# Kernel optimization log

Hardware: AMD Instinct MI355X
Metric: run time of the kernel (lower is better)

The kernel has to match this reference:

```python
import jax, jax.numpy as jnp
import numpy as np

B, T, D = 2, 2048, 2048
H, DH, DR, DL = 16, 128, 64, 512
WINDOW, STRIDE, GLOBAL = 512, 64, 128
BASE, MAX_SEQ, ORIG_MAX = 10000.0, 131072, 4096
BETA_FAST, BETA_SLOW = 32.0, 1.0
SCALE = 1.0 / np.sqrt(DH)
SCALE_ROPE = 1.0 / np.sqrt(DR)


def _yarn_inv_freq():
    base_inv = 1.0 / (BASE ** (np.arange(0, DR, 2, dtype=np.float32) / DR))
    scale = MAX_SEQ / ORIG_MAX
    freqs = np.arange(DR // 2, dtype=np.float32)
    ramp = np.clip((freqs - BETA_SLOW) / (BETA_FAST - BETA_SLOW), 0.0, 1.0)
    return jnp.asarray(base_inv * (1 - ramp) + (base_inv / scale) * ramp)

_INV_FREQ = _yarn_inv_freq()
_YARN_FACTOR = np.float32(0.1 * np.log(MAX_SEQ / ORIG_MAX) + 1.0)


def _apply_rope(x):
    # x: [B, H, T, DR]
    t = jnp.arange(x.shape[2], dtype=jnp.float32)
    fr = t[:, None] * _INV_FREQ[None, :]            # [T, DR/2]
    emb = jnp.concatenate([fr, fr], axis=-1)        # [T, DR]
    cos, sin = jnp.cos(emb), jnp.sin(emb)
    x1, x2 = jnp.split(x, 2, axis=-1)
    rot = jnp.concatenate([-x2, x1], axis=-1)
    return (x * cos + rot * sin) * _YARN_FACTOR


def _sparse_mask(seq_len):
    pos = jnp.arange(seq_len)
    qp, kp = pos[:, None], pos[None, :]
    dist = qp - kp
    half = WINDOW // 2
    window = (dist >= -half) & (dist <= half)
    dilated = (kp % STRIDE == 0) | (kp < GLOBAL)
    causal = kp <= qp
    return (window | dilated) & causal              # [T, T] bool


def setup_inputs() -> dict:
    key = jax.random.key(0)
    ks = jax.random.split(key, 9)
    s = 0.02
    return {
        "x": jax.random.normal(ks[0], (B, T, D), jnp.float32),
        "w_q": jax.random.normal(ks[1], (D, D), jnp.float32) * s,
        "w_dkv": jax.random.normal(ks[2], (D, DL), jnp.float32) * s,
        "w_uk": jax.random.normal(ks[3], (DL, D), jnp.float32) * s,
        "w_uv": jax.random.normal(ks[4], (DL, D), jnp.float32) * s,
        "w_q_pos": jax.random.normal(ks[5], (D, H * DR), jnp.float32) * s,
        "w_k_pos": jax.random.normal(ks[6], (D, H * DR), jnp.float32) * s,
        "w_o": jax.random.normal(ks[7], (D, D), jnp.float32) * s,
    }


def reference(x, w_q, w_dkv, w_uk, w_uv, w_q_pos, w_k_pos, w_o):
    b, t, _ = x.shape
    # MLA projections
    q_c = (x @ w_q).reshape(b, t, H, DH).transpose(0, 2, 1, 3)      # [B,H,T,DH]
    c_kv = x @ w_dkv                                                # [B,T,DL]
    k_c = (c_kv @ w_uk).reshape(b, t, H, DH).transpose(0, 2, 1, 3)
    v_c = (c_kv @ w_uv).reshape(b, t, H, DH).transpose(0, 2, 1, 3)
    # decoupled RoPE branch (YaRN)
    q_r = (x @ w_q_pos).reshape(b, t, H, DR).transpose(0, 2, 1, 3)
    k_r = (x @ w_k_pos).reshape(b, t, H, DR).transpose(0, 2, 1, 3)
    q_r = _apply_rope(q_r)
    k_r = _apply_rope(k_r)
    # combined content + positional scores
    scores = jnp.einsum("bhqd,bhkd->bhqk", q_c, k_c) * SCALE \
           + jnp.einsum("bhqr,bhkr->bhqk", q_r, k_r) * SCALE_ROPE
    mask = _sparse_mask(t)                                          # [T,T]
    scores = jnp.where(mask[None, None], scores, -jnp.inf)
    attn = jax.nn.softmax(scores, axis=-1)
    out = jnp.einsum("bhqk,bhkd->bhqd", attn, v_c)                  # [B,H,T,DH]
    out = out.transpose(0, 2, 1, 3).reshape(b, t, D)
    return out @ w_o
```

## Files before the change

kernel.cpp:

```cpp
#include <hip/hip_runtime.h>
#include <hip/hip_bf16.h>
#include <cstdint>

typedef __attribute__((ext_vector_type(8))) short short8_t;
typedef __attribute__((ext_vector_type(4))) short short4_t;
typedef __attribute__((ext_vector_type(4))) float f32x4_t;

#define AS1 __attribute__((address_space(1)))
#define AS3 __attribute__((address_space(3)))

__device__ __forceinline__ void gload_lds16(const void* g, void* l) {
  __builtin_amdgcn_global_load_lds((const AS1 void*)g, (AS3 void*)l, 16, 0, 0);
}

__device__ __forceinline__ short8_t ld8(const __hip_bfloat16* p) {
  return *(const short8_t*)p;
}

__global__ __launch_bounds__(256) void k_convert(const float* __restrict__ in,
                                                 __hip_bfloat16* __restrict__ out, int n) {
  int i = (blockIdx.x * 256 + threadIdx.x) * 8;
  if (i >= n) return;
  union { short8_t v; __hip_bfloat16 h[8]; } u;
#pragma unroll
  for (int j = 0; j < 8; ++j) u.h[j] = __float2bfloat16(in[i + j]);
  *(short8_t*)(out + i) = u.v;
}

__global__ __launch_bounds__(256) void k_transpose(const float* __restrict__ in,
                                                   __hip_bfloat16* __restrict__ out,
                                                   int R, int C) {
  __shared__ float t[64][65];
  int nct = C >> 6;
  int ct = blockIdx.x % nct, rt = blockIdx.x / nct;
  int r0 = rt << 6, c0 = ct << 6;
#pragma unroll
  for (int i = 0; i < 16; ++i) {
    int idx = i * 256 + threadIdx.x;
    int r = idx >> 6, c = idx & 63;
    t[r][c] = in[(size_t)(r0 + r) * C + c0 + c];
  }
  __syncthreads();
#pragma unroll
  for (int i = 0; i < 16; ++i) {
    int idx = i * 256 + threadIdx.x;
    int c = idx >> 6, r = idx & 63;
    out[(size_t)(c0 + c) * R + r0 + r] = __float2bfloat16(t[r][c]);
  }
}

template<int OUT_F32>
__global__ __launch_bounds__(256) void k_gemm_bt(const __hip_bfloat16* __restrict__ A,
                                                 const __hip_bfloat16* __restrict__ Bt,
                                                 void* __restrict__ C,
                                                 int M, int N, int K, float alpha) {
  __shared__ __align__(16) __hip_bfloat16 Al[128 * 32];
  __shared__ __align__(16) __hip_bfloat16 Bl[128 * 32];
  int nbx = N >> 7;
  int bx = blockIdx.x % nbx, by = blockIdx.x / nbx;
  int tid = threadIdx.x, lane = tid & 63, w = tid >> 6;
  int wr = (w >> 1) << 6, wc = (w & 1) << 6;
  f32x4_t acc[4][4] = {};
  const __hip_bfloat16* Ag = A + (size_t)(by * 128) * K;
  const __hip_bfloat16* Bg = Bt + (size_t)(bx * 128) * K;
  int srow = w * 32 + (lane >> 2);
  int scol = (lane & 3) * 8;
  for (int k0 = 0; k0 < K; k0 += 32) {
    __syncthreads();
    gload_lds16(Ag + (size_t)srow * K + k0 + scol,        Al + (w * 32) * 32);
    gload_lds16(Ag + (size_t)(srow + 16) * K + k0 + scol, Al + (w * 32 + 16) * 32);
    gload_lds16(Bg + (size_t)srow * K + k0 + scol,        Bl + (w * 32) * 32);
    gload_lds16(Bg + (size_t)(srow + 16) * K + k0 + scol, Bl + (w * 32 + 16) * 32);
    __syncthreads();
    short8_t af[4], bf[4];
#pragma unroll
    for (int m = 0; m < 4; ++m)
      af[m] = ld8(Al + (wr + 16 * m + (lane & 15)) * 32 + 8 * (lane >> 4));
#pragma unroll
    for (int n = 0; n < 4; ++n)
      bf[n] = ld8(Bl + (wc + 16 * n + (lane & 15)) * 32 + 8 * (lane >> 4));
#pragma unroll
    for (int m = 0; m < 4; ++m)
#pragma unroll
      for (int n = 0; n < 4; ++n)
        acc[m][n] = __builtin_amdgcn_mfma_f32_16x16x32_bf16(af[m], bf[n], acc[m][n], 0, 0, 0);
  }
  int r0 = by * 128 + wr + 4 * (lane >> 4);
  int c0 = bx * 128 + wc + (lane & 15);
#pragma unroll
  for (int m = 0; m < 4; ++m)
#pragma unroll
    for (int n = 0; n < 4; ++n)
#pragma unroll
      for (int i = 0; i < 4; ++i) {
        size_t o = (size_t)(r0 + 16 * m + i) * N + c0 + 16 * n;
        float v = acc[m][n][i] * alpha;
        if (OUT_F32) ((float*)C)[o] = v;
        else ((__hip_bfloat16*)C)[o] = __float2bfloat16(v);
      }
}

__global__ __launch_bounds__(256) void k_gemm_proj1(const __hip_bfloat16* __restrict__ A,
                                                    const __hip_bfloat16* __restrict__ Bt,
                                                    __hip_bfloat16* __restrict__ qcb,
                                                    __hip_bfloat16* __restrict__ qrb,
                                                    __hip_bfloat16* __restrict__ krb,
                                                    __hip_bfloat16* __restrict__ ckv) {
  const int K = 2048;
  __shared__ __align__(16) __hip_bfloat16 Al[128 * 32];
  __shared__ __align__(16) __hip_bfloat16 Bl[128 * 32];
  int bx = blockIdx.x % 36, by = blockIdx.x / 36;
  int tid = threadIdx.x, lane = tid & 63, w = tid >> 6;
  int L = lane & 15, hi = lane >> 4;
  int wr = (w >> 1) << 6, wc = (w & 1) << 6;
  f32x4_t acc[4][4] = {};
  const __hip_bfloat16* Ag = A + (size_t)(by * 128) * K;
  const __hip_bfloat16* Bg = Bt + (size_t)(bx * 128) * K;
  int srow = w * 32 + (lane >> 2);
  int scol = (lane & 3) * 8;
  for (int k0 = 0; k0 < K; k0 += 32) {
    __syncthreads();
    gload_lds16(Ag + (size_t)srow * K + k0 + scol,        Al + (w * 32) * 32);
    gload_lds16(Ag + (size_t)(srow + 16) * K + k0 + scol, Al + (w * 32 + 16) * 32);
    gload_lds16(Bg + (size_t)srow * K + k0 + scol,        Bl + (w * 32) * 32);
    gload_lds16(Bg + (size_t)(srow + 16) * K + k0 + scol, Bl + (w * 32 + 16) * 32);
    __syncthreads();
    short8_t af[4], bf[4];
#pragma unroll
    for (int m = 0; m < 4; ++m)
      af[m] = ld8(Al + (wr + 16 * m + L) * 32 + 8 * hi);
#pragma unroll
    for (int n = 0; n < 4; ++n)
      bf[n] = ld8(Bl + (wc + 16 * n + L) * 32 + 8 * hi);
#pragma unroll
    for (int m = 0; m < 4; ++m)
#pragma unroll
      for (int n = 0; n < 4; ++n)
        acc[m][n] = __builtin_amdgcn_mfma_f32_16x16x32_bf16(af[m], bf[n], acc[m][n], 0, 0, 0);
  }
  int r0 = by * 128 + wr + 4 * hi;
  int cb = bx * 128 + wc;
  if (bx < 16) {
    const float SCALE = 0.08838834764831845f;
#pragma unroll
    for (int m = 0; m < 4; ++m)
#pragma unroll
      for (int n = 0; n < 4; ++n)
#pragma unroll
        for (int i = 0; i < 4; ++i)
          qcb[(size_t)(r0 + 16 * m + i) * 2048 + cb + 16 * n + L] =
              __float2bfloat16(acc[m][n][i] * SCALE);
  } else if (bx < 32) {
    bool isq = bx < 24;
    __hip_bfloat16* dst = isq ? qrb : krb;
    float osc = isq ? 0.16832169878499666f : 1.3465735902799727f;
    int cbl = cb - (isq ? 2048 : 3072);
    float invf[2];
#pragma unroll
    for (int p = 0; p < 2; ++p) {
      float fi = (float)(16 * p + L);
      float bi = __expf(fi * -0.28782313662425574f);
      float ramp = fminf(fmaxf((fi - 1.0f) * (1.0f / 31.0f), 0.0f), 1.0f);
      invf[p] = bi * (1.0f - ramp * (31.0f / 32.0f));
    }
#pragma unroll
    for (int m = 0; m < 4; ++m)
#pragma unroll
      for (int i = 0; i < 4; ++i) {
        int row = r0 + 16 * m + i;
        float ft = (float)(row & 2047);
#pragma unroll
        for (int p = 0; p < 2; ++p) {
          float sn, cs;
          __sincosf(ft * invf[p], &sn, &cs);
          float x1 = acc[m][p][i], x2 = acc[m][p + 2][i];
          dst[(size_t)row * 1024 + cbl + 16 * p + L] =
              __float2bfloat16((x1 * cs - x2 * sn) * osc);
          dst[(size_t)row * 1024 + cbl + 32 + 16 * p + L] =
              __float2bfloat16((x2 * cs + x1 * sn) * osc);
        }
      }
  } else {
    int cbl = cb - 4096;
#pragma unroll
    for (int m = 0; m < 4; ++m)
#pragma unroll
      for (int n = 0; n < 4; ++n)
#pragma unroll
        for (int i = 0; i < 4; ++i)
          ckv[(size_t)(r0 + 16 * m + i) * 512 + cbl + 16 * n + L] =
              __float2bfloat16(acc[m][n][i]);
  }
}

__global__ __launch_bounds__(256) void k_gemm_proj2(const __hip_bfloat16* __restrict__ A,
                                                    const __hip_bfloat16* __restrict__ Bt,
                                                    __hip_bfloat16* __restrict__ kcb,
                                                    __hip_bfloat16* __restrict__ vcb,
                                                    __hip_bfloat16* __restrict__ vT) {
  const int K = 512;
  __shared__ __align__(16) __hip_bfloat16 Al[128 * 32];
  __shared__ __align__(16) __hip_bfloat16 Bl[128 * 32];
  int bx = blockIdx.x & 31, by = blockIdx.x >> 5;
  int tid = threadIdx.x, lane = tid & 63, w = tid >> 6;
  int L = lane & 15, hi = lane >> 4;
  int wr = (w >> 1) << 6, wc = (w & 1) << 6;
  f32x4_t acc[4][4] = {};
  const __hip_bfloat16* Ag = A + (size_t)(by * 128) * K;
  const __hip_bfloat16* Bg = Bt + (size_t)(bx * 128) * K;
  int srow = w * 32 + (lane >> 2);
  int scol = (lane & 3) * 8;
  for (int k0 = 0; k0 < K; k0 += 32) {
    __syncthreads();
    gload_lds16(Ag + (size_t)srow * K + k0 + scol,        Al + (w * 32) * 32);
    gload_lds16(Ag + (size_t)(srow + 16) * K + k0 + scol, Al + (w * 32 + 16) * 32);
    gload_lds16(Bg + (size_t)srow * K + k0 + scol,        Bl + (w * 32) * 32);
    gload_lds16(Bg + (size_t)(srow + 16) * K + k0 + scol, Bl + (w * 32 + 16) * 32);
    __syncthreads();
    short8_t af[4], bf[4];
#pragma unroll
    for (int m = 0; m < 4; ++m)
      af[m] = ld8(Al + (wr + 16 * m + L) * 32 + 8 * hi);
#pragma unroll
    for (int n = 0; n < 4; ++n)
      bf[n] = ld8(Bl + (wc + 16 * n + L) * 32 + 8 * hi);
#pragma unroll
    for (int m = 0; m < 4; ++m)
#pragma unroll
      for (int n = 0; n < 4; ++n)
        acc[m][n] = __builtin_amdgcn_mfma_f32_16x16x32_bf16(af[m], bf[n], acc[m][n], 0, 0, 0);
  }
  int r0 = by * 128 + wr + 4 * hi;
  int cb = bx * 128 + wc;
  if (bx < 16) {
#pragma unroll
    for (int m = 0; m < 4; ++m)
#pragma unroll
      for (int n = 0; n < 4; ++n)
#pragma unroll
        for (int i = 0; i < 4; ++i)
          kcb[(size_t)(r0 + 16 * m + i) * 2048 + cb + 16 * n + L] =
              __float2bfloat16(acc[m][n][i]);
  } else {
#pragma unroll
    for (int m = 0; m < 4; ++m)
#pragma unroll
      for (int n = 0; n < 4; ++n) {
        int vcol = cb - 2048 + 16 * n + L;
        int hh = vcol >> 7, dh = vcol & 127;
        int row0 = r0 + 16 * m;
        int b = row0 >> 11, t0 = row0 & 2047;
        union { short4_t v; __hip_bfloat16 h4[4]; } pk;
#pragma unroll
        for (int i = 0; i < 4; ++i) {
          __hip_bfloat16 bv = __float2bfloat16(acc[m][n][i]);
          vcb[(size_t)(row0 + i) * 2048 + vcol] = bv;
          pk.h4[i] = bv;
        }
        *(short4_t*)(vT + ((size_t)((b * 16 + hh) * 128 + dh) * 2048 + t0)) = pk.v;
      }
  }
}

__global__ __launch_bounds__(256) void k_attn(const __hip_bfloat16* __restrict__ qc,
                                              const __hip_bfloat16* __restrict__ kc,
                                              const __hip_bfloat16* __restrict__ vcb,
                                              const __hip_bfloat16* __restrict__ qr,
                                              const __hip_bfloat16* __restrict__ kr,
                                              const __hip_bfloat16* __restrict__ vT,
                                              __hip_bfloat16* __restrict__ ao) {
  const int T = 2048;
  int bid = blockIdx.x;
  int xcd = bid & 7, r = bid >> 3;
  int j = r >> 5, qt = r & 31;
  int bh = xcd + 8 * j;
  int b = bh >> 4, h = bh & 15;
  int tid = threadIdx.x, lane = tid & 63, w = tid >> 6;
  int L = lane & 15, hi = lane >> 4;
  int q0 = qt * 64;

  __shared__ __align__(16) __hip_bfloat16 Kl[64 * 200];
  __shared__ __align__(16) __hip_bfloat16 Vt[128 * 64];
  __shared__ __align__(16) __hip_bfloat16 Pl[4][16 * 72];

  char* Vtb = (char*)Vt;
  const __hip_bfloat16* vTb = vT + (size_t)(b * 16 + h) * 128 * 2048;

  int qrow = q0 + w * 16 + L;
  size_t qb = (size_t)b * T + qrow;
  short8_t qf[6];
#pragma unroll
  for (int c = 0; c < 4; ++c)
    qf[c] = ld8(qc + qb * 2048 + h * 128 + 32 * c + 8 * hi);
#pragma unroll
  for (int c = 0; c < 2; ++c)
    qf[4 + c] = ld8(qr + qb * 1024 + h * 64 + 32 * c + 8 * hi);

  f32x4_t oacc[8] = {};
  float mrow[4], lrow[4];
#pragma unroll
  for (int i = 0; i < 4; ++i) { mrow[i] = -1e30f; lrow[i] = 0.0f; }

  int nd = qt - 6;

  for (int step = 0; step <= qt + 1; ++step) {
    bool compact = (step == qt + 1);
    if (compact && nd <= 0) break;
    int kt = step;
    if (!compact && kt > 1 && kt < qt - 4) continue;
    int k0 = kt * 64;

    if (!compact) {
#pragma unroll
      for (int i = 0; i < 6; ++i) {
        int ch = i * 256 + tid;
        int rr = ch / 24;
        int d = (ch % 24) * 8;
        size_t krow = (size_t)b * T + k0 + rr;
        const __hip_bfloat16* src = (d < 128)
            ? kc + krow * 2048 + h * 128 + d
            : kr + krow * 1024 + h * 64 + (d - 128);
        *(short8_t*)(Kl + rr * 200 + d) = ld8(src);
      }
#pragma unroll
      for (int i = 0; i < 4; ++i) {
        int ch = i * 256 + tid;
        int row = ch >> 3, c = ch & 7;
        int swc = c ^ (row & 7);
        *(short8_t*)(Vtb + row * 128 + 16 * swc) = ld8(vTb + (size_t)row * 2048 + k0 + c * 8);
      }
    } else {
#pragma unroll
      for (int i = 0; i < 6; ++i) {
        int ch = i * 256 + tid;
        int rr = ch / 24;
        int d = (ch % 24) * 8;
        int srcr = (rr < nd) ? 64 * (2 + rr) : 0;
        size_t krow = (size_t)b * T + srcr;
        const __hip_bfloat16* src = (d < 128)
            ? kc + krow * 2048 + h * 128 + d
            : kr + krow * 1024 + h * 64 + (d - 128);
        *(short8_t*)(Kl + rr * 200 + d) = ld8(src);
      }
#pragma unroll
      for (int i = 0; i < 2; ++i) {
        int ch = i * 256 + tid;
        int jj = ch >> 4, d0 = (ch & 15) * 8;
        if (jj < nd) {
          union { short8_t v; __hip_bfloat16 hh[8]; } u;
          u.v = ld8(vcb + (size_t)(b * 2048 + 64 * (2 + jj)) * 2048 + h * 128 + d0);
#pragma unroll
          for (int q = 0; q < 8; ++q) {
            int dh = d0 + q;
            int swc = (jj >> 3) ^ (dh & 7);
            *(__hip_bfloat16*)(Vtb + dh * 128 + 16 * swc + 2 * (jj & 7)) = u.hh[q];
          }
        }
      }
    }
    __syncthreads();

    f32x4_t sacc[4] = {};
    __builtin_amdgcn_s_setprio(1);
#pragma unroll
    for (int n = 0; n < 4; ++n)
#pragma unroll
      for (int c = 0; c < 6; ++c) {
        short8_t bfr = ld8(Kl + (16 * n + L) * 200 + 32 * c + 8 * hi);
        sacc[n] = __builtin_amdgcn_mfma_f32_16x16x32_bf16(qf[c], bfr, sacc[n], 0, 0, 0);
      }
    __builtin_amdgcn_s_setprio(0);

    int rbase = q0 + w * 16 + 4 * hi;
    float p[4][4];
    float mt[4];
#pragma unroll
    for (int i = 0; i < 4; ++i) mt[i] = -1e30f;
#pragma unroll
    for (int n = 0; n < 4; ++n) {
      int col = L + 16 * n;
      int k = k0 + col;
#pragma unroll
      for (int i = 0; i < 4; ++i) {
        int rq = rbase + i;
        bool ok = compact ? (col < nd)
                          : ((k <= rq) && ((rq - k <= 256) || ((k & 63) == 0) || (k < 128)));
        float s = ok ? sacc[n][i] : -1e30f;
        p[n][i] = s;
        mt[i] = fmaxf(mt[i], s);
      }
    }
    for (int d = 1; d < 16; d <<= 1)
#pragma unroll
      for (int i = 0; i < 4; ++i) mt[i] = fmaxf(mt[i], __shfl_xor(mt[i], d, 64));
    float al[4], rs[4];
#pragma unroll
    for (int i = 0; i < 4; ++i) {
      float mnew = fmaxf(mrow[i], mt[i]);
      al[i] = __expf(mrow[i] - mnew);
      mrow[i] = mnew;
      rs[i] = 0.0f;
    }
#pragma unroll
    for (int n = 0; n < 4; ++n)
#pragma unroll
      for (int i = 0; i < 4; ++i) {
        float e = __expf(p[n][i] - mrow[i]);
        p[n][i] = e;
        rs[i] += e;
      }
    for (int d = 1; d < 16; d <<= 1)
#pragma unroll
      for (int i = 0; i < 4; ++i) rs[i] += __shfl_xor(rs[i], d, 64);
#pragma unroll
    for (int i = 0; i < 4; ++i) lrow[i] = lrow[i] * al[i] + rs[i];
#pragma unroll
    for (int n = 0; n < 8; ++n)
#pragma unroll
      for (int i = 0; i < 4; ++i) oacc[n][i] *= al[i];

#pragma unroll
    for (int n = 0; n < 4; ++n)
#pragma unroll
      for (int i = 0; i < 4; ++i)
        Pl[w][(4 * hi + i) * 72 + 16 * n + L] = __float2bfloat16(p[n][i]);
    __syncthreads();

    __builtin_amdgcn_s_setprio(1);
#pragma unroll
    for (int ks = 0; ks < 2; ++ks) {
      short8_t pa = ld8(Pl[w] + L * 72 + 32 * ks + 8 * hi);
#pragma unroll
      for (int n = 0; n < 8; ++n) {
        int vrow = 16 * n + L;
        int chunk = (4 * ks + hi) ^ (vrow & 7);
        short8_t bv = *(const short8_t*)(Vtb + vrow * 128 + 16 * chunk);
        oacc[n] = __builtin_amdgcn_mfma_f32_16x16x32_bf16(pa, bv, oacc[n], 0, 0, 0);
      }
    }
    __builtin_amdgcn_s_setprio(0);
    __syncthreads();
  }

#pragma unroll
  for (int n = 0; n < 8; ++n)
#pragma unroll
    for (int i = 0; i < 4; ++i) {
      int rq = q0 + w * 16 + 4 * hi + i;
      int cdh = 16 * n + L;
      float v = oacc[n][i] / lrow[i];
      ao[((size_t)b * T + rq) * 2048 + h * 128 + cdh] = __float2bfloat16(v);
    }
}

extern "C" void kernel_launch(void* const* d_in, const int* in_sizes, int n_in,
                              void* d_out, int out_size, void* d_ws, size_t ws_size,
                              hipStream_t stream) {
  const float* x     = (const float*)d_in[0];
  const float* w_q   = (const float*)d_in[1];
  const float* w_dkv = (const float*)d_in[2];
  const float* w_uk  = (const float*)d_in[3];
  const float* w_uv  = (const float*)d_in[4];
  const float* w_qp  = (const float*)d_in[5];
  const float* w_kp  = (const float*)d_in[6];
  const float* w_o   = (const float*)d_in[7];
  float* out = (float*)d_out;

  char* ws = (char*)d_ws;
  size_t off = 0;
  auto alloc = [&](size_t elems) {
    __hip_bfloat16* p = (__hip_bfloat16*)(ws + off);
    off += ((elems * 2 + 255) & ~(size_t)255);
    return p;
  };
  __hip_bfloat16* xb  = alloc(8388608);
  __hip_bfloat16* Bt1 = alloc(4608UL * 2048);
  __hip_bfloat16* Bt2 = alloc(4096UL * 512);
  __hip_bfloat16* woT = alloc(4194304);
  __hip_bfloat16* qcb = alloc(8388608);
  __hip_bfloat16* ckv = alloc(2097152);
  __hip_bfloat16* kcb = alloc(8388608);
  __hip_bfloat16* vcb = alloc(8388608);
  __hip_bfloat16* qrb = alloc(4194304);
  __hip_bfloat16* krb = alloc(4194304);
  __hip_bfloat16* aob = alloc(8388608);
  __hip_bfloat16* vT  = alloc(8388608);

  k_convert<<<4096, 256, 0, stream>>>(x, xb, 8388608);
  k_transpose<<<32 * 32, 256, 0, stream>>>(w_q,   Bt1,               2048, 2048);
  k_transpose<<<32 * 16, 256, 0, stream>>>(w_qp,  Bt1 + 2048UL * 2048, 2048, 1024);
  k_transpose<<<32 * 16, 256, 0, stream>>>(w_kp,  Bt1 + 3072UL * 2048, 2048, 1024);
  k_transpose<<<32 * 8,  256, 0, stream>>>(w_dkv, Bt1 + 4096UL * 2048, 2048, 512);
  k_transpose<<<8 * 32,  256, 0, stream>>>(w_uk,  Bt2,               512, 2048);
  k_transpose<<<8 * 32,  256, 0, stream>>>(w_uv,  Bt2 + 2048UL * 512, 512, 2048);
  k_transpose<<<32 * 32, 256, 0, stream>>>(w_o,   woT,               2048, 2048);

  k_gemm_proj1<<<36 * 32, 256, 0, stream>>>(xb, Bt1, qcb, qrb, krb, ckv);
  k_gemm_proj2<<<32 * 32, 256, 0, stream>>>(ckv, Bt2, kcb, vcb, vT);

  k_attn<<<1024, 256, 0, stream>>>(qcb, kcb, vcb, qrb, krb, vT, aob);

  k_gemm_bt<1><<<32 * 16, 256, 0, stream>>>(aob, woT, out, 4096, 2048, 2048, 1.0f);
}
```

Before: 299.1 us.

## Unify GEMMs into 4-stage pipelined kernel with XCD-aware block remapping

Replaces the three separate bf16 GEMM kernels with one templated kernel. It uses a 4-deep LDS ring buffer with async global-to-LDS loads issued three tiles ahead, and explicit vmcnt waits with one barrier per k-step. Block IDs are remapped so consecutive tiles land on the same XCD for better L2 reuse, and MFMA sections get raised priority. LDS use grows fourfold (64KB per block), which may reduce occupancy.

Measured after the change: 302.1 us. No clear change (+1.0%).

```diff
diff --git a/kernel.cpp b/kernel.cpp
--- a/kernel.cpp
+++ b/kernel.cpp
@@ -49,216 +49,163 @@
   }
 }
 
-template<int OUT_F32>
-__global__ __launch_bounds__(256) void k_gemm_bt(const __hip_bfloat16* __restrict__ A,
-                                                 const __hip_bfloat16* __restrict__ Bt,
-                                                 void* __restrict__ C,
-                                                 int M, int N, int K, float alpha) {
-  __shared__ __align__(16) __hip_bfloat16 Al[128 * 32];
-  __shared__ __align__(16) __hip_bfloat16 Bl[128 * 32];
-  int nbx = N >> 7;
-  int bx = blockIdx.x % nbx, by = blockIdx.x / nbx;
-  int tid = threadIdx.x, lane = tid & 63, w = tid >> 6;
-  int wr = (w >> 1) << 6, wc = (w & 1) << 6;
-  f32x4_t acc[4][4] = {};
-  const __hip_bfloat16* Ag = A + (size_t)(by * 128) * K;
-  const __hip_bfloat16* Bg = Bt + (size_t)(bx * 128) * K;
-  int srow = w * 32 + (lane >> 2);
-  int scol = (lane & 3) * 8;
-  for (int k0 = 0; k0 < K; k0 += 32) {
-    __syncthreads();
-    gload_lds16(Ag + (size_t)srow * K + k0 + scol,        Al + (w * 32) * 32);
-    gload_lds16(Ag + (size_t)(srow + 16) * K + k0 + scol, Al + (w * 32 + 16) * 32);
-    gload_lds16(Bg + (size_t)srow * K + k0 + scol,        Bl + (w * 32) * 32);
-    gload_lds16(Bg + (size_t)(srow + 16) * K + k0 + scol, Bl + (w * 32 + 16) * 32);
-    __syncthreads();
-    short8_t af[4], bf[4];
-#pragma unroll
-    for (int m = 0; m < 4; ++m)
-      af[m] = ld8(Al + (wr + 16 * m + (lane & 15)) * 32 + 8 * (lane >> 4));
-#pragma unroll
-    for (int n = 0; n < 4; ++n)
-      bf[n] = ld8(Bl + (wc + 16 * n + (lane & 15)) * 32 + 8 * (lane >> 4));
-#pragma unroll
-    for (int m = 0; m < 4; ++m)
-#pragma unroll
-      for (int n = 0; n < 4; ++n)
-        acc[m][n] = __builtin_amdgcn_mfma_f32_16x16x32_bf16(af[m], bf[n], acc[m][n], 0, 0, 0);
-  }
-  int r0 = by * 128 + wr + 4 * (lane >> 4);
-  int c0 = bx * 128 + wc + (lane & 15);
-#pragma unroll
-  for (int m = 0; m < 4; ++m)
-#pragma unroll
-    for (int n = 0; n < 4; ++n)
-#pragma unroll
-      for (int i = 0; i < 4; ++i) {
-        size_t o = (size_t)(r0 + 16 * m + i) * N + c0 + 16 * n;
-        float v = acc[m][n][i] * alpha;
-        if (OUT_F32) ((float*)C)[o] = v;
-        else ((__hip_bfloat16*)C)[o] = __float2bfloat16(v);
-      }
-}
-
-__global__ __launch_bounds__(256) void k_gemm_proj1(const __hip_bfloat16* __restrict__ A,
-                                                    const __hip_bfloat16* __restrict__ Bt,
-                                                    __hip_bfloat16* __restrict__ qcb,
-                                                    __hip_bfloat16* __restrict__ qrb,
-                                                    __hip_bfloat16* __restrict__ krb,
-                                                    __hip_bfloat16* __restrict__ ckv) {
-  const int K = 2048;
-  __shared__ __align__(16) __hip_bfloat16 Al[128 * 32];
-  __shared__ __align__(16) __hip_bfloat16 Bl[128 * 32];
-  int bx = blockIdx.x % 36, by = blockIdx.x / 36;
+template<int MODE>
+__global__ __launch_bounds__(256) void k_gemm2(const __hip_bfloat16* __restrict__ A,
+                                               const __hip_bfloat16* __restrict__ Bt,
+                                               int K, int nbx,
+                                               void* __restrict__ O0, void* __restrict__ O1,
+                                               void* __restrict__ O2, void* __restrict__ O3,
+                                               float alpha) {
+  __shared__ __align__(16) __hip_bfloat16 Al[4][128 * 32];
+  __shared__ __align__(16) __hip_bfloat16 Bl[4][128 * 32];
+  int q = gridDim.x >> 3;
+  int id = blockIdx.x;
+  int sid = (id & 7) * q + (id >> 3);
+  int bx = sid % nbx, by = sid / nbx;
   int tid = threadIdx.x, lane = tid & 63, w = tid >> 6;
   int L = lane & 15, hi = lane >> 4;
   int wr = (w >> 1) << 6, wc = (w & 1) << 6;
   f32x4_t acc[4][4] = {};
   const __hip_bfloat16* Ag = A + (size_t)(by * 128) * K;
   const __hip_bfloat16* Bg = Bt + (size_t)(bx * 128) * K;
-  int srow = w * 32 + (lane >> 2);
-  int scol = (lane & 3) * 8;
-  for (int k0 = 0; k0 < K; k0 += 32) {
-    __syncthreads();
-    gload_lds16(Ag + (size_t)srow * K + k0 + scol,        Al + (w * 32) * 32);
-    gload_lds16(Ag + (size_t)(srow + 16) * K + k0 + scol, Al + (w * 32 + 16) * 32);
-    gload_lds16(Bg + (size_t)srow * K + k0 + scol,        Bl + (w * 32) * 32);
-    gload_lds16(Bg + (size_t)(srow + 16) * K + k0 + scol, Bl + (w * 32 + 16) * 32);
-    __syncthreads();
+  int rA = w * 16 + (lane >> 2);
+  int cA = (lane & 3) * 8;
+  int NT = K >> 5;
+
+  auto stage = [&](int s) {
+    int j = s & 3;
+    int k0 = s << 5;
+    gload_lds16(Ag + (size_t)rA * K + k0 + cA,        &Al[j][(w * 16) * 32]);
+    gload_lds16(Ag + (size_t)(rA + 64) * K + k0 + cA, &Al[j][(64 + w * 16) * 32]);
+    gload_lds16(Bg + (size_t)rA * K + k0 + cA,        &Bl[j][(w * 16) * 32]);
+    gload_lds16(Bg + (size_t)(rA + 64) * K + k0 + cA, &Bl[j][(64 + w * 16) * 32]);
+  };
+
+  stage(0); stage(1); stage(2);
+  asm volatile("s_waitcnt vmcnt(8)\ns_barrier" ::: "memory");
+
+  for (int t = 0; t < NT; ++t) {
+    int j = t & 3;
     short8_t af[4], bf[4];
 #pragma unroll
-    for (int m = 0; m < 4; ++m)
-      af[m] = ld8(Al + (wr + 16 * m + L) * 32 + 8 * hi);
-#pragma unroll
-    for (int n = 0; n < 4; ++n)
-      bf[n] = ld8(Bl + (wc + 16 * n + L) * 32 + 8 * hi);
+    for (int m = 0; m < 4; ++m) af[m] = ld8(&Al[j][(wr + 16 * m + L) * 32 + 8 * hi]);
+#pragma unroll
+    for (int n = 0; n < 4; ++n) bf[n] = ld8(&Bl[j][(wc + 16 * n + L) * 32 + 8 * hi]);
+    int rem = NT - t;
+    if (rem >= 4) stage(t + 3);
+    __builtin_amdgcn_s_setprio(1);
 #pragma unroll
     for (int m = 0; m < 4; ++m)
 #pragma unroll
       for (int n = 0; n < 4; ++n)
         acc[m][n] = __builtin_amdgcn_mfma_f32_16x16x32_bf16(af[m], bf[n], acc[m][n], 0, 0, 0);
+    __builtin_amdgcn_s_setprio(0);
+    if (rem >= 4)      asm volatile("s_waitcnt vmcnt(8)\ns_barrier" ::: "memory");
+    else if (rem == 3) asm volatile("s_waitcnt vmcnt(4)\ns_barrier" ::: "memory");
+    else if (rem == 2) asm volatile("s_waitcnt vmcnt(0)\ns_barrier" ::: "memory");
   }
+
   int r0 = by * 128 + wr + 4 * hi;
   int cb = bx * 128 + wc;
-  if (bx < 16) {
-    const float SCALE = 0.08838834764831845f;
+
+  if (MODE == 1) {
+    float* C = (float*)O0;
+    size_t N = (size_t)nbx << 7;
 #pragma unroll
     for (int m = 0; m < 4; ++m)
 #pragma unroll
       for (int n = 0; n < 4; ++n)
 #pragma unroll
         for (int i = 0; i < 4; ++i)
-          qcb[(size_t)(r0 + 16 * m + i) * 2048 + cb + 16 * n + L] =
-              __float2bfloat16(acc[m][n][i] * SCALE);
-  } else if (bx < 32) {
-    bool isq = bx < 24;
-    __hip_bfloat16* dst = isq ? qrb : krb;
-    float osc = isq ? 0.16832169878499666f : 1.3465735902799727f;
-    int cbl = cb - (isq ? 2048 : 3072);
-    float invf[2];
-#pragma unroll
-    for (int p = 0; p < 2; ++p) {
-      float fi = (float)(16 * p + L);
-      float bi = __expf(fi * -0.28782313662425574f);
-      float ramp = fminf(fmaxf((fi - 1.0f) * (1.0f / 31.0f), 0.0f), 1.0f);
-      invf[p] = bi * (1.0f - ramp * (31.0f / 32.0f));
-    }
-#pragma unroll
-    for (int m = 0; m < 4; ++m)
-#pragma unroll
-      for (int i = 0; i < 4; ++i) {
-        int row = r0 + 16 * m + i;
-        float ft = (float)(row & 2047);
-#pragma unroll
-        for (int p = 0; p < 2; ++p) {
-          float sn, cs;
-          __sincosf(ft * invf[p], &sn, &cs);
-          float x1 = acc[m][p][i], x2 = acc[m][p + 2][i];
-          dst[(size_t)row * 1024 + cbl + 16 * p + L] =
-              __float2bfloat16((x1 * cs - x2 * sn) * osc);
-          dst[(size_t)row * 1024 + cbl + 32 + 16 * p + L] =
-              __float2bfloat16((x2 * cs + x1 * sn) * osc);
+          C[(size_t)(r0 + 16 * m + i) * N + cb + 16 * n + L] = acc[m][n][i] * alpha;
+  } else if (MODE == 2) {
+    __hip_bfloat16* qcb = (__hip_bfloat16*)O0;
+    __hip_bfloat16* qrb = (__hip_bfloat16*)O1;
+    __hip_bfloat16* krb = (__hip_bfloat16*)O2;
+    __hip_bfloat16* ckv = (__hip_bfloat16*)O3;
+    if (bx < 16) {
+      const float SCALE = 0.08838834764831845f;
+#pragma unroll
+      for (int m = 0; m < 4; ++m)
+#pragma unroll
+        for (int n = 0; n < 4; ++n)
+#pragma unroll
+          for (int i = 0; i < 4; ++i)
+            qcb[(size_t)(r0 + 16 * m + i) * 2048 + cb + 16 * n + L] =
+                __float2bfloat16(acc[m][n][i] * SCALE);
+    } else if (bx < 32) {
+      bool isq = bx < 24;
+      __hip_bfloat16* dst = isq ? qrb : krb;
+      float osc = isq ? 0.16832169878499666f : 1.3465735902799727f;
+      int cbl = cb - (isq ? 2048 : 3072);
+      float invf[2];
+#pragma unroll
+      for (int p = 0; p < 2; ++p) {
+        float fi = (float)(16 * p + L);
+        float bi = __expf(fi * -0.28782313662425574f);
+        float ramp = fminf(fmaxf((fi - 1.0f) * (1.0f / 31.0f), 0.0f), 1.0f);
+        invf[p] = bi * (1.0f - ramp * (31.0f / 32.0f));
+      }
+#pragma unroll
+      for (int m = 0; m < 4; ++m)
+#pragma unroll
+        for (int i = 0; i < 4; ++i) {
+          int row = r0 + 16 * m + i;
+          float ft = (float)(row & 2047);
+#pragma unroll
+          for (int p = 0; p < 2; ++p) {
+            float sn, cs;
+            __sincosf(ft * invf[p], &sn, &cs);
+            float x1 = acc[m][p][i], x2 = acc[m][p + 2][i];
+            dst[(size_t)row * 1024 + cbl + 16 * p + L] =
+                __float2bfloat16((x1 * cs - x2 * sn) * osc);
+            dst[(size_t)row * 1024 + cbl + 32 + 16 * p + L] =
+                __float2bfloat16((x2 * cs + x1 * sn) * osc);
+          }
         }
-      }
-  } else {
-    int cbl = cb - 4096;
-#pragma unroll
-    for (int m = 0; m < 4; ++m)
-#pragma unroll
-      for (int n = 0; n < 4; ++n)
-#pragma unroll
-        for (int i = 0; i < 4; ++i)
-          ckv[(size_t)(r0 + 16 * m + i) * 512 + cbl + 16 * n + L] =
-              __float2bfloat16(acc[m][n][i]);
-  }
-}
-
-__global__ __launch_bounds__(256) void k_gemm_proj2(const __hip_bfloat16* __restrict__ A,
-                                                    const __hip_bfloat16* __restrict__ Bt,
-                                                    __hip_bfloat16* __restrict__ kcb,
-                                                    __hip_bfloat16* __restrict__ vcb,
-                                                    __hip_bfloat16* __restrict__ vT) {
-  const int K = 512;
-  __shared__ __align__(16) __hip_bfloat16 Al[128 * 32];
-  __shared__ __align__(16) __hip_bfloat16 Bl[128 * 32];
-  int bx = blockIdx.x & 31, by = blockIdx.x >> 5;
-  int tid = threadIdx.x, lane = tid & 63, w = tid >> 6;
-  int L = lane & 15, hi = lane >> 4;
-  int wr = (w >> 1) << 6, wc = (w & 1) << 6;
-  f32x4_t acc[4][4] = {};
-  const __hip_bfloat16* Ag = A + (size_t)(by * 128) * K;
-  const __hip_bfloat16* Bg = Bt + (size_t)(bx * 128) * K;
-  int srow = w * 32 + (lane >> 2);
-  int scol = (lane & 3) * 8;
-  for (int k0 = 0; k0 < K; k0 += 32) {
-    __syncthreads();
-    gload_lds16(Ag + (size_t)srow * K + k0 + scol,        Al + (w * 32) * 32);
-    gload_lds16(Ag + (size_t)(srow + 16) * K + k0 + scol, Al + (w * 32 + 16) * 32);
-    gload_lds16(Bg + (size_t)srow * K + k0 + scol,        Bl + (w * 32) * 32);
-    gload_lds16(Bg + (size_t)(srow + 16) * K + k0 + scol, Bl + (w * 32 + 16) * 32);
-    __syncthreads();
-    short8_t af[4], bf[4];
-#pragma unroll
-    for (int m = 0; m < 4; ++m)
-      af[m] = ld8(Al + (wr + 16 * m + L) * 32 + 8 * hi);
-#pragma unroll
-    for (int n = 0; n < 4; ++n)
-      bf[n] = ld8(Bl + (wc + 16 * n + L) * 32 + 8 * hi);
-#pragma unroll
-    for (int m = 0; m < 4; ++m)
-#pragma unroll
-      for (int n = 0; n < 4; ++n)
-        acc[m][n] = __builtin_amdgcn_mfma_f32_16x16x32_bf16(af[m], bf[n], acc[m][n], 0, 0, 0);
-  }
-  int r0 = by * 128 + wr + 4 * hi;
-  int cb = bx * 128 + wc;
-  if (bx < 16) {
-#pragma unroll
-    for (int m = 0; m < 4; ++m)
-#pragma unroll
-      for (int n = 0; n < 4; ++n)
-#pragma unroll
-        for (int i = 0; i < 4; ++i)
-          kcb[(size_t)(r0 + 16 * m + i) * 2048 + cb + 16 * n + L] =
-              __float2bfloat16(acc[m][n][i]);
-  } else {
-#pragma unroll
-    for (int m = 0; m < 4; ++m)
-#pragma unroll
-      for (int n = 0; n < 4; ++n) {
-        int vcol = cb - 2048 + 16 * n + L;
-        int hh = vcol >> 7, dh = vcol & 127;
-        int row0 = r0 + 16 * m;
-        int b = row0 >> 11, t0 = row0 & 2047;
-        union { short4_t v; __hip_bfloat16 h4[4]; } pk;
-#pragma unroll
-        for (int i = 0; i < 4; ++i) {
-          __hip_bfloat16 bv = __float2bfloat16(acc[m][n][i]);
-          vcb[(size_t)(row0 + i) * 2048 + vcol] = bv;
-          pk.h4[i] = bv;
+    } else {
+      int cbl = cb - 4096;
+#pragma unroll
+      for (int m = 0; m < 4; ++m)
+#pragma unroll
+        for (int n = 0; n < 4; ++n)
+#pragma unroll
+          for (int i = 0; i < 4; ++i)
+            ckv[(size_t)(r0 + 16 * m + i) * 512 + cbl + 16 * n + L] =
+                __float2bfloat16(acc[m][n][i]);
+    }
+  } else if (MODE == 3) {
+    __hip_bfloat16* kcb = (__hip_bfloat16*)O0;
+    __hip_bfloat16* vcb = (__hip_bfloat16*)O1;
+    __hip_bfloat16* vT  = (__hip_bfloat16*)O2;
+    if (bx < 16) {
+#pragma unroll
+      for (int m = 0; m < 4; ++m)
+#pragma unroll
+        for (int n = 0; n < 4; ++n)
+#pragma unroll
+          for (int i = 0; i < 4; ++i)
+            kcb[(size_t)(r0 + 16 * m + i) * 2048 + cb + 16 * n + L] =
+                __float2bfloat16(acc[m][n][i]);
+    } else {
+#pragma unroll
+      for (int m = 0; m < 4; ++m)
+#pragma unroll
+        for (int n = 0; n < 4; ++n) {
+          int vcol = cb - 2048 + 16 * n + L;
+          int hh = vcol >> 7, dh = vcol & 127;
+          int row0 = r0 + 16 * m;
+          int b = row0 >> 11, t0 = row0 & 2047;
+          union { short4_t v; __hip_bfloat16 h4[4]; } pk;
+#pragma unroll
+          for (int i = 0; i < 4; ++i) {
+            __hip_bfloat16 bv = __float2bfloat16(acc[m][n][i]);
+            vcb[(size_t)(row0 + i) * 2048 + vcol] = bv;
+            pk.h4[i] = bv;
+          }
+          *(short4_t*)(vT + ((size_t)((b * 16 + hh) * 128 + dh) * 2048 + t0)) = pk.v;
         }
-        *(short4_t*)(vT + ((size_t)((b * 16 + hh) * 128 + dh) * 2048 + t0)) = pk.v;
-      }
+    }
   }
 }
 
@@ -350,10 +297,10 @@
           union { short8_t v; __hip_bfloat16 hh[8]; } u;
           u.v = ld8(vcb + (size_t)(b * 2048 + 64 * (2 + jj)) * 2048 + h * 128 + d0);
 #pragma unroll
-          for (int q = 0; q < 8; ++q) {
-            int dh = d0 + q;
+          for (int qq = 0; qq < 8; ++qq) {
+            int dh = d0 + qq;
             int swc = (jj >> 3) ^ (dh & 7);
-            *(__hip_bfloat16*)(Vtb + dh * 128 + 16 * swc + 2 * (jj & 7)) = u.hh[q];
+            *(__hip_bfloat16*)(Vtb + dh * 128 + 16 * swc + 2 * (jj & 7)) = u.hh[qq];
           }
         }
       }
@@ -487,18 +434,18 @@
   __hip_bfloat16* vT  = alloc(8388608);
 
   k_convert<<<4096, 256, 0, stream>>>(x, xb, 8388608);
-  k_transpose<<<32 * 32, 256, 0, stream>>>(w_q,   Bt1,               2048, 2048);
+  k_transpose<<<32 * 32, 256, 0, stream>>>(w_q,   Bt1,                 2048, 2048);
   k_transpose<<<32 * 16, 256, 0, stream>>>(w_qp,  Bt1 + 2048UL * 2048, 2048, 1024);
   k_transpose<<<32 * 16, 256, 0, stream>>>(w_kp,  Bt1 + 3072UL * 2048, 2048, 1024);
   k_transpose<<<32 * 8,  256, 0, stream>>>(w_dkv, Bt1 + 4096UL * 2048, 2048, 512);
-  k_transpose<<<8 * 32,  256, 0, stream>>>(w_uk,  Bt2,               512, 2048);
-  k_transpose<<<8 * 32,  256, 0, stream>>>(w_uv,  Bt2 + 2048UL * 512, 512, 2048);
-  k_transpose<<<32 * 32, 256, 0, stream>>>(w_o,   woT,               2048, 2048);
-
-  k_gemm_proj1<<<36 * 32, 256, 0, stream>>>(xb, Bt1, qcb, qrb, krb, ckv);
-  k_gemm_proj2<<<32 * 32, 256, 0, stream>>>(ckv, Bt2, kcb, vcb, vT);
+  k_transpose<<<8 * 32,  256, 0, stream>>>(w_uk,  Bt2,                 512, 2048);
+  k_transpose<<<8 * 32,  256, 0, stream>>>(w_uv,  Bt2 + 2048UL * 512,  512, 2048);
+  k_transpose<<<32 * 32, 256, 0, stream>>>(w_o,   woT,                 2048, 2048);
+
+  k_gemm2<2><<<36 * 32, 256, 0, stream>>>(xb, Bt1, 2048, 36, qcb, qrb, krb, ckv, 1.0f);
+  k_gemm2<3><<<32 * 32, 256, 0, stream>>>(ckv, Bt2, 512, 32, kcb, vcb, vT, nullptr, 1.0f);
 
   k_attn<<<1024, 256, 0, stream>>>(qcb, kcb, vcb, qrb, krb, vT, aob);
 
-  k_gemm_bt<1><<<32 * 16, 256, 0, stream>>>(aob, woT, out, 4096, 2048, 2048, 1.0f);
-}
+  k_gemm2<1><<<16 * 32, 256, 0, stream>>>(aob, woT, 2048, 16, out, nullptr, nullptr, nullptr, 1.0f);
+}
```
